# Kernel tuning notes

Measured on AMD Instinct MI355X. Metric: run time of the kernel, lower is better.

The kernel has to match this reference:

```python
import jax, jax.numpy as jnp
import numpy as np
from jax.ops import segment_sum, segment_max

N = 20000; E = 320000; IN_F = 135; HID = 256; HEADS = 8; DH = HID // HEADS; L = 4
EPS = 1e-5; TOP_K = max(1, int(N * 0.2)); POWER = 3.0

def lrelu(x):
    return jnp.where(x >= 0, x, 0.2 * x)

def bn_eval(x, p):
    # p rows: gamma, beta, running_mean, running_var (eval-mode BatchNorm1d)
    return p[0] * (x - p[2]) * jax.lax.rsqrt(p[3] + EPS) + p[1]

def setup_inputs():
    key = jax.random.key(0)
    ks = iter(jax.random.split(key, 100))
    def rn(shape, s=0.05):
        return jax.random.normal(next(ks), shape, jnp.float32) * s
    def bn_p(c):
        g = jax.random.uniform(next(ks), (c,)) * 0.5 + 0.75
        v = jax.random.uniform(next(ks), (c,)) * 0.5 + 0.75
        return jnp.stack([g, rn((c,), 0.1), rn((c,), 0.1), v])
    return dict(
        x=jax.random.normal(next(ks), (N, IN_F), jnp.float32),
        edge_index=jax.random.randint(next(ks), (2, E), 0, N),
        cen_W=rn((32, 7), 0.3), cen_b=rn((32,)), cen_bn=bn_p(32),
        emb_W=rn((64, 128), 0.1), emb_b=rn((64,)), emb_bn=bn_p(64),
        fus_W=rn((64, 96), 0.1), fus_b=rn((64,)),
        fa_W1=rn((64, 64), 0.1), fa_b1=rn((64,)),
        fa_W2=rn((64, 64), 0.1), fa_b2=rn((64,)),
        adj_W=rn((HID, 64), 0.1), adj_b=rn((HID,)),
        gcn_W=rn((L, HID, HID), 0.06), gcn_b=rn((L, HID)),
        gat_W=rn((L, HID, HID), 0.06), gat_b=rn((L, HID)),
        gat_asrc=rn((L, HEADS, DH), 0.1), gat_adst=rn((L, HEADS, DH), 0.1),
        layer_bn=jnp.stack([bn_p(HID) for _ in range(L)]),
        gate_W=rn((L, HID), 0.1), gate_b=rn((L,)),
        lin1_W=rn((HID, HID * L), 0.03), lin1_b=rn((HID,)),
        mlp_W1=rn((2 * HID, HID), 0.06), mlp_b1=rn((2 * HID,)), mlp_bn1=bn_p(2 * HID),
        mlp_W2=rn((HID, 2 * HID), 0.04), mlp_b2=rn((HID,)), mlp_bn2=bn_p(HID),
        mlp_W3=rn((1, HID), 0.06), mlp_b3=rn((1,)),
        temperature=jnp.array([0.05], jnp.float32),
    )

def _forward(edge_index, x, cen_W, cen_b, cen_bn, emb_W, emb_b, emb_bn, fus_W, fus_b,
             fa_W1, fa_b1, fa_W2, fa_b2, adj_W, adj_b, gcn_W, gcn_b, gat_W, gat_b,
             gat_asrc, gat_adst, layer_bn, gate_W, gate_b, lin1_W, lin1_b,
             mlp_W1, mlp_b1, mlp_bn1, mlp_W2, mlp_b2, mlp_bn2, mlp_W3, mlp_b3, temperature):
    # --- add self-loops (GCNConv and GATConv both do this by default) ---
    loops = jnp.arange(N)
    src = jnp.concatenate([edge_index[0], loops])  # [E+N]
    dst = jnp.concatenate([edge_index[1], loops])
    deg = segment_sum(jnp.ones(E + N, jnp.float32), dst, num_segments=N)
    dinv = jax.lax.rsqrt(deg)  # deg >= 1 because of self-loops
    gcn_norm = dinv[src] * dinv[dst]  # [E+N]

    # --- FeatureFusionLayer (eval BN) ---
    c = bn_eval(lrelu(x[:, :7] @ cen_W.T + cen_b), cen_bn)        # [N,32]
    e = bn_eval(lrelu(x[:, 7:] @ emb_W.T + emb_b), emb_bn)        # [N,64]
    h = jnp.concatenate([c, e], axis=1) @ fus_W.T + fus_b         # [N,64]
    att = jax.nn.sigmoid(lrelu(h @ fa_W1.T + fa_b1) @ fa_W2.T + fa_b2)
    h = (h * att) @ adj_W.T + adj_b                               # [N,256]

    xs = []
    prev = h
    cur = h
    for i in range(L):
        # GCNConv: D^{-1/2}(A+I)D^{-1/2} X W + b
        g = cur @ gcn_W[i].T                                      # [N,256]
        cur = segment_sum(g[src] * gcn_norm[:, None], dst, num_segments=N) + gcn_b[i]
        # GATConv: per-edge attention with segment softmax over destinations
        hh = (cur @ gat_W[i].T).reshape(N, HEADS, DH)             # [N,8,32]
        a_s = jnp.sum(hh * gat_asrc[i], axis=-1)                  # [N,8]
        a_d = jnp.sum(hh * gat_adst[i], axis=-1)
        logits = lrelu(a_s[src] + a_d[dst])                       # [E+N,8]
        mx = segment_max(logits, dst, num_segments=N)
        ex = jnp.exp(logits - mx[dst])
        den = segment_sum(ex, dst, num_segments=N)
        alpha = ex / den[dst]                                     # [E+N,8]
        cur = segment_sum(alpha[:, :, None] * hh[src], dst, num_segments=N)
        cur = cur.reshape(N, HID) + gat_b[i]
        # BN -> LeakyReLU -> sigmoid-gated residual (dropout = identity in eval)
        cur = lrelu(bn_eval(cur, layer_bn[i]))
        gate = jax.nn.sigmoid(cur @ gate_W[i] + gate_b[i])[:, None]
        cur = gate * cur + (1.0 - gate) * prev
        prev = cur
        xs.append(cur)

    jk = jnp.concatenate(xs, axis=1)                              # [N, 1024]
    h2 = lrelu(jk @ lin1_W.T + lin1_b)
    m1 = bn_eval(lrelu(h2 @ mlp_W1.T + mlp_b1), mlp_bn1)
    m2 = bn_eval(lrelu(m1 @ mlp_W2.T + mlp_b2), mlp_bn2)
    raw = jax.nn.sigmoid(m2 @ mlp_W3.T + mlp_b3)[:, 0]           # [N]

    # ContrastEnhancementLayer (eval path)
    scaled = raw / temperature[0]
    enhanced = jax.nn.softmax(scaled, axis=0)
    threshold = jax.lax.top_k(scaled, TOP_K)[0][-1]               # k-th largest
    mask = (scaled >= threshold).astype(scaled.dtype)
    boosted = enhanced * (mask + 0.1 * (1.0 - mask))
    return boosted ** POWER

def reference(x, edge_index, cen_W, cen_b, cen_bn, emb_W, emb_b, emb_bn, fus_W, fus_b,
              fa_W1, fa_b1, fa_W2, fa_b2, adj_W, adj_b, gcn_W, gcn_b, gat_W, gat_b,
              gat_asrc, gat_adst, layer_bn, gate_W, gate_b, lin1_W, lin1_b,
              mlp_W1, mlp_b1, mlp_bn1, mlp_W2, mlp_b2, mlp_bn2, mlp_W3, mlp_b3, temperature):
    return _forward(edge_index, x, cen_W, cen_b, cen_bn, emb_W, emb_b, emb_bn, fus_W, fus_b,
                    fa_W1, fa_b1, fa_W2, fa_b2, adj_W, adj_b, gcn_W, gcn_b, gat_W, gat_b,
                    gat_asrc, gat_adst, layer_bn, gate_W, gate_b, lin1_W, lin1_b,
                    mlp_W1, mlp_b1, mlp_bn1, mlp_W2, mlp_b2, mlp_bn2, mlp_W3, mlp_b3, temperature)
```

## Files before the change

### kernel.cpp

```cpp
#include <hip/hip_runtime.h>
#include <hip/hip_bf16.h>
#include <stdint.h>
#include <stddef.h>

#define NN    20000
#define EE    320000
#define ENE   340000
#define HIDD  256
#define TOPKK 4000

__device__ __forceinline__ float d_lrelu(float x){ return x >= 0.0f ? x : 0.2f * x; }
__device__ __forceinline__ float d_sig(float x){ return 1.0f / (1.0f + expf(-x)); }
__device__ __forceinline__ double d_sig64(double x){ return 1.0 / (1.0 + exp(-x)); }
__device__ __forceinline__ unsigned long long d_key64(double x){
  unsigned long long u = (unsigned long long)__double_as_longlong(x);
  return (u & 0x8000000000000000ULL) ? ~u : (u | 0x8000000000000000ULL);
}

__global__ void kf_fdet(const unsigned* __restrict__ xw, int* __restrict__ fflag){
  int t = threadIdx.x;
  unsigned w = xw[t * 101 + 7];
  unsigned b = (w >> 8) & 0x7F;
  int isbf = (b >= 0x3Au && b <= 0x44u) ? 1 : 0;
  unsigned long long bal = __ballot(isbf);
  if (t == 0) fflag[0] = (__popcll(bal) >= 32) ? 1 : 0;
}

__global__ void kf_cvt(const void* __restrict__ src, const int* __restrict__ fflag,
                       float* __restrict__ dst, int n){
  int stride = gridDim.x * 256;
  int bf = fflag[0];
  for (int i = blockIdx.x * 256 + threadIdx.x; i < n; i += stride){
    if (bf){
      unsigned short u = ((const unsigned short*)src)[i];
      dst[i] = __uint_as_float(((unsigned)u) << 16);
    } else {
      dst[i] = ((const float*)src)[i];
    }
  }
}

struct CvtTab { const void* src[34]; int cnt[34]; int off[34]; };
__global__ void kf_cvtw(CvtTab tab, const int* __restrict__ fflag, float* __restrict__ wbuf){
  int i = blockIdx.y;
  int n = tab.cnt[i];
  int idx = blockIdx.x * 256 + threadIdx.x;
  if (idx >= n) return;
  int bf = fflag[0];
  float v;
  if (bf){
    unsigned short u = ((const unsigned short*)tab.src[i])[idx];
    v = __uint_as_float(((unsigned)u) << 16);
  } else {
    v = ((const float*)tab.src[i])[idx];
  }
  wbuf[tab.off[i] + idx] = v;
}

__global__ void kf_cnt13(const int* __restrict__ ei, unsigned* __restrict__ C){
  __shared__ unsigned loc[6];
  if (threadIdx.x < 6) loc[threadIdx.x] = 0;
  __syncthreads();
  for (int e = blockIdx.x * 256 + threadIdx.x; e < EE; e += gridDim.x * 256){
    int s1 = ei[e], d1 = ei[EE + e];
    if (s1 >= 0 && s1 < NN && d1 >= 0 && d1 < NN) atomicAdd(&loc[0], 1u);
    if (s1 == 0) atomicAdd(&loc[1], 1u);
    if (d1 == 0) atomicAdd(&loc[2], 1u);
    int s3 = ei[2 * e], d3 = ei[2 * e + 1];
    if (s3 >= 0 && s3 < NN && d3 >= 0 && d3 < NN) atomicAdd(&loc[3], 1u);
    if (s3 == 0) atomicAdd(&loc[4], 1u);
    if (d3 == 0) atomicAdd(&loc[5], 1u);
  }
  __syncthreads();
  if (threadIdx.x < 6) atomicAdd(&C[threadIdx.x], loc[threadIdx.x]);
}

__global__ void kf_dec13(const unsigned* __restrict__ C, int* __restrict__ esel){
  const unsigned zlim = EE / 64;
  bool h1 = (C[0] == EE) && (C[1] < zlim) && (C[2] < zlim);
  bool h3 = (C[3] == EE) && (C[4] < zlim) && (C[5] < zlim);
  esel[0] = h1 ? 1 : (h3 ? 3 : -1);
}

__global__ void kf_cnt02(const int* __restrict__ ei, const int* __restrict__ esel,
                         unsigned* __restrict__ C){
  if (esel[0] >= 0) return;
  const long long* q = (const long long*)ei;
  __shared__ unsigned loc[6];
  if (threadIdx.x < 6) loc[threadIdx.x] = 0;
  __syncthreads();
  for (int e = blockIdx.x * 256 + threadIdx.x; e < EE; e += gridDim.x * 256){
    long long s0 = q[e], d0 = q[EE + e];
    if (s0 >= 0 && s0 < NN && d0 >= 0 && d0 < NN) atomicAdd(&loc[0], 1u);
    if (s0 == 0) atomicAdd(&loc[1], 1u);
    if (d0 == 0) atomicAdd(&loc[2], 1u);
    long long s2 = q[2 * e], d2 = q[2 * e + 1];
    if (s2 >= 0 && s2 < NN && d2 >= 0 && d2 < NN) atomicAdd(&loc[3], 1u);
    if (s2 == 0) atomicAdd(&loc[4], 1u);
    if (d2 == 0) atomicAdd(&loc[5], 1u);
  }
  __syncthreads();
  if (threadIdx.x < 6) atomicAdd(&C[threadIdx.x], loc[threadIdx.x]);
}

__global__ void kf_dec02(const unsigned* __restrict__ C13, const unsigned* __restrict__ C02,
                         int* __restrict__ esel){
  if (esel[0] >= 0){ esel[1] = 0; return; }
  const unsigned zlim = EE / 64;
  bool h0 = (C02[0] == EE) && (C02[1] < zlim) && (C02[2] < zlim);
  bool h2 = (C02[3] == EE) && (C02[4] < zlim) && (C02[5] < zlim);
  if (h0){ esel[0] = 0; esel[1] = 0; }
  else if (h2){ esel[0] = 2; esel[1] = 0; }
  else { esel[0] = -9; esel[1] = 1; }
}

__global__ void kf_econv(const int* __restrict__ ei, const int* __restrict__ esel,
                         int* __restrict__ src_i, int* __restrict__ dst_i){
  int e = blockIdx.x * 256 + threadIdx.x;
  if (e >= ENE) return;
  if (e >= EE){ src_i[e] = e - EE; dst_i[e] = e - EE; return; }
  int sel = esel[0];
  const long long* q = (const long long*)ei;
  int s, d;
  if (sel == 0){ s = (int)q[e]; d = (int)q[EE + e]; }
  else if (sel == 1){ s = ei[e]; d = ei[EE + e]; }
  else if (sel == 2){ s = (int)q[2 * e]; d = (int)q[2 * e + 1]; }
  else if (sel == 3){ s = ei[2 * e]; d = ei[2 * e + 1]; }
  else { s = 0; d = 0; }
  src_i[e] = s; dst_i[e] = d;
}

__global__ void kf_deg(const int* __restrict__ dst_i, int* __restrict__ deg){
  int e = blockIdx.x * 256 + threadIdx.x;
  if (e < ENE) atomicAdd(&deg[dst_i[e]], 1);
}

__global__ __launch_bounds__(1024) void kf_scan(const int* __restrict__ deg,
                                                int* __restrict__ rowptr,
                                                float* __restrict__ dinv){
  __shared__ int buf[1024];
  const int CH = (NN + 1023) / 1024;
  int t = threadIdx.x;
  int base = t * CH;
  int s = 0;
  for (int j = 0; j < CH; ++j){
    int v = base + j;
    if (v < NN) s += deg[v];
  }
  buf[t] = s;
  __syncthreads();
  int val = s;
  for (int d = 1; d < 1024; d <<= 1){
    int add = (t >= d) ? buf[t - d] : 0;
    __syncthreads();
    buf[t] += add;
    __syncthreads();
  }
  int run = buf[t] - val;
  for (int j = 0; j < CH; ++j){
    int v = base + j;
    if (v < NN){
      rowptr[v] = run;
      run += deg[v];
      dinv[v] = 1.0f / sqrtf((float)deg[v]);
    }
  }
  if (t == 1023) rowptr[NN] = buf[1023];
}

__global__ void kf_fill(const int* __restrict__ src_i, const int* __restrict__ dst_i,
                        const int* __restrict__ rowptr, int* __restrict__ fill,
                        int* __restrict__ col){
  int e = blockIdx.x * 256 + threadIdx.x;
  if (e >= ENE) return;
  int d = dst_i[e];
  int p = atomicAdd(&fill[d], 1);
  col[rowptr[d] + p] = src_i[e];
}

__global__ void kf_sort(const int* __restrict__ rowptr, int* __restrict__ col){
  int v = blockIdx.x * 256 + threadIdx.x;
  if (v >= NN) return;
  int b = rowptr[v], e = rowptr[v + 1];
  for (int i = b + 1; i < e; ++i){
    int key = col[i];
    int j = i - 1;
    while (j >= b && col[j] > key){ col[j + 1] = col[j]; --j; }
    col[j + 1] = key;
  }
}

template<int EP>
__global__ __launch_bounds__(256) void kgf(
    const float* __restrict__ A, int lda,
    const float* __restrict__ W, int ldw,
    const float* __restrict__ bias,
    const float* __restrict__ bn,
    const float* __restrict__ mul,
    float* __restrict__ C, int ldc,
    int M, int K, int F)
{
  __shared__ float As[16][68];
  __shared__ float Ws[16][68];
  int tid  = threadIdx.x;
  int row0 = blockIdx.x * 64;
  int col0 = blockIdx.y * 64;
  int tx = tid & 15, ty = tid >> 4;
  int lr  = tid >> 2;
  int lk4 = (tid & 3) * 4;
  float acc[4][4] = {};
  int r_st = row0 + lr;
  int f_st = col0 + lr;
  for (int k0 = 0; k0 < K; k0 += 16){
#pragma unroll
    for (int j = 0; j < 4; ++j){
      int k = k0 + lk4 + j;
      As[lk4 + j][lr] = (r_st < M && k < K) ? A[(size_t)r_st * lda + k] : 0.0f;
      Ws[lk4 + j][lr] = (f_st < F && k < K) ? W[(size_t)f_st * ldw + k] : 0.0f;
    }
    __syncthreads();
#pragma unroll
    for (int kk = 0; kk < 16; ++kk){
      float av[4], bv[4];
#pragma unroll
      for (int i = 0; i < 4; ++i){ av[i] = As[kk][ty * 4 + i]; bv[i] = Ws[kk][tx * 4 + i]; }
#pragma unroll
      for (int i = 0; i < 4; ++i)
#pragma unroll
        for (int j = 0; j < 4; ++j)
          acc[i][j] = fmaf(av[i], bv[j], acc[i][j]);
    }
    __syncthreads();
  }
#pragma unroll
  for (int i = 0; i < 4; ++i){
    int r = row0 + ty * 4 + i;
    if (r >= M) continue;
#pragma unroll
    for (int j = 0; j < 4; ++j){
      int f = col0 + tx * 4 + j;
      if (f >= F) continue;
      float z = acc[i][j];
      size_t ci = (size_t)r * ldc + f;
      if (EP == 0){
        if (bias) z += bias[f];
        C[ci] = z;
      } else if (EP == 1){
        C[ci] = d_lrelu(z + bias[f]);
      } else if (EP == 2){
        z = d_lrelu(z + bias[f]);
        float gamma = bn[f], beta = bn[F + f], mean = bn[2 * F + f], var = bn[3 * F + f];
        C[ci] = gamma * (z - mean) * (1.0f / sqrtf(var + 1e-5f)) + beta;
      } else if (EP == 3){
        z += bias[f];
        C[ci] = d_sig(z) * mul[(size_t)r * ldc + f];
      } else if (EP == 4){
        C[ci] += z;
      } else {
        C[ci] = d_lrelu(C[ci] + z + bias[f]);
      }
    }
  }
}

__global__ __launch_bounds__(256) void kf_gcn(const float* __restrict__ g,
                                              const int* __restrict__ rowptr,
                                              const int* __restrict__ col,
                                              const float* __restrict__ dinv,
                                              const float* __restrict__ bias,
                                              float* __restrict__ out){
  int lane = threadIdx.x & 63, wid = threadIdx.x >> 6;
  int v = blockIdx.x * 4 + wid;
  if (v >= NN) return;
  float dv = dinv[v];
  float a0 = 0.f, a1 = 0.f, a2 = 0.f, a3 = 0.f;
  int e0 = rowptr[v], e1 = rowptr[v + 1];
  for (int e = e0; e < e1; ++e){
    int s = col[e];
    float w = dinv[s] * dv;
    const float* gr = g + (size_t)s * HIDD + lane;
    a0 = fmaf(w, gr[0],   a0);
    a1 = fmaf(w, gr[64],  a1);
    a2 = fmaf(w, gr[128], a2);
    a3 = fmaf(w, gr[192], a3);
  }
  float* o = out + (size_t)v * HIDD + lane;
  o[0]   = a0 + bias[lane];
  o[64]  = a1 + bias[lane + 64];
  o[128] = a2 + bias[lane + 128];
  o[192] = a3 + bias[lane + 192];
}

__global__ __launch_bounds__(256) void kf_asd(const float* __restrict__ hh,
                                              const float* __restrict__ asrc,
                                              const float* __restrict__ adst,
                                              float* __restrict__ a_s,
                                              float* __restrict__ a_d){
  int lane = threadIdx.x & 63, wid = threadIdx.x >> 6;
  int v = blockIdx.x * 4 + wid;
  if (v >= NN) return;
  int h = lane >> 3;
  int d0 = (lane & 7) * 4;
  const float* x = hh + (size_t)v * HIDD + h * 32 + d0;
  float ps = 0.f, pd = 0.f;
#pragma unroll
  for (int j = 0; j < 4; ++j){
    ps = fmaf(x[j], asrc[h * 32 + d0 + j], ps);
    pd = fmaf(x[j], adst[h * 32 + d0 + j], pd);
  }
#pragma unroll
  for (int off = 1; off < 8; off <<= 1){
    ps += __shfl_xor(ps, off);
    pd += __shfl_xor(pd, off);
  }
  if ((lane & 7) == 0){
    a_s[v * 8 + h] = ps;
    a_d[v * 8 + h] = pd;
  }
}

__global__ __launch_bounds__(256) void kf_gat(const float* __restrict__ hh,
                                              const int* __restrict__ rowptr,
                                              const int* __restrict__ col,
                                              const float* __restrict__ a_s,
                                              const float* __restrict__ a_d,
                                              float* __restrict__ elog,
                                              const float* __restrict__ gat_b,
                                              const float* __restrict__ lbn,
                                              const float* __restrict__ gate_W,
                                              const float* __restrict__ gate_b,
                                              float* __restrict__ P){
  int lane = threadIdx.x & 63, wid = threadIdx.x >> 6;
  int v = blockIdx.x * 4 + wid;
  if (v >= NN) return;
  int head = lane & 7, slot = lane >> 3;
  int e0 = rowptr[v], e1 = rowptr[v + 1];
  float adv = a_d[v * 8 + head];
  float m = -1e30f;
  for (int e = e0 + slot; e < e1; e += 8){
    float lg = d_lrelu(a_s[col[e] * 8 + head] + adv);
    m = fmaxf(m, lg);
  }
#pragma unroll
  for (int off = 8; off < 64; off <<= 1) m = fmaxf(m, __shfl_xor(m, off));
  float s = 0.f;
  for (int e = e0 + slot; e < e1; e += 8){
    float ex = expf(d_lrelu(a_s[col[e] * 8 + head] + adv) - m);
    elog[(size_t)e * 8 + head] = ex;
    s += ex;
  }
#pragma unroll
  for (int off = 8; off < 64; off <<= 1) s += __shfl_xor(s, off);
  int hk[4]; float denk[4];
#pragma unroll
  for (int k = 0; k < 4; ++k){
    int f = lane + 64 * k;
    hk[k] = f >> 5;
    denk[k] = __shfl(s, hk[k]);
  }
  float acc[4] = {0.f, 0.f, 0.f, 0.f};
  for (int e = e0; e < e1; ++e){
    const float* hr = hh + (size_t)col[e] * HIDD;
#pragma unroll
    for (int k = 0; k < 4; ++k)
      acc[k] = fmaf(elog[(size_t)e * 8 + hk[k]], hr[lane + 64 * k], acc[k]);
  }
  float o[4], gp = 0.f;
#pragma unroll
  for (int k = 0; k < 4; ++k){
    int f = lane + 64 * k;
    float z = acc[k] / denk[k] + gat_b[f];
    float gamma = lbn[f], beta = lbn[256 + f], mean = lbn[512 + f], var = lbn[768 + f];
    z = gamma * (z - mean) * (1.0f / sqrtf(var + 1e-5f)) + beta;
    z = d_lrelu(z);
    o[k] = z;
    gp = fmaf(z, gate_W[f], gp);
  }
#pragma unroll
  for (int off = 1; off < 64; off <<= 1) gp += __shfl_xor(gp, off);
  float gate = d_sig(gp + gate_b[0]);
#pragma unroll
  for (int k = 0; k < 4; ++k){
    size_t idx = (size_t)v * HIDD + lane + 64 * k;
    P[idx] = gate * o[k] + (1.0f - gate) * P[idx];
  }
}

__global__ __launch_bounds__(256) void kf_raw(const float* __restrict__ m2,
                                              const float* __restrict__ W3,
                                              const float* __restrict__ b3,
                                              const float* __restrict__ temp,
                                              double* __restrict__ scaled){
  int lane = threadIdx.x & 63, wid = threadIdx.x >> 6;
  int v = blockIdx.x * 4 + wid;
  if (v >= NN) return;
  const float* r = m2 + (size_t)v * HIDD;
  double s = 0.;
#pragma unroll
  for (int k = 0; k < 4; ++k) s = fma((double)r[lane + 64 * k], (double)W3[lane + 64 * k], s);
#pragma unroll
  for (int off = 1; off < 64; off <<= 1) s += __shfl_xor(s, off);
  if (lane == 0) scaled[v] = d_sig64(s + (double)b3[0]) / (double)temp[0];
}

__global__ __launch_bounds__(1024) void kf_stats(const double* __restrict__ scaled,
                                                 double* __restrict__ st){
  __shared__ double fmx[1024];
  __shared__ double dsum[1024];
  int t = threadIdx.x;
  double m = -1e300;
  for (int i = t; i < NN; i += 1024) m = fmax(m, scaled[i]);
  fmx[t] = m;
  __syncthreads();
  for (int d = 512; d > 0; d >>= 1){
    if (t < d) fmx[t] = fmax(fmx[t], fmx[t + d]);
    __syncthreads();
  }
  double mx = fmx[0];
  double s = 0.;
  for (int i = t; i < NN; i += 1024) s += exp(scaled[i] - mx);
  dsum[t] = s;
  __syncthreads();
  for (int d = 512; d > 0; d >>= 1){
    if (t < d) dsum[t] += dsum[t + d];
    __syncthreads();
  }
  if (t == 0){ st[0] = mx; st[1] = dsum[0]; }
}

__global__ __launch_bounds__(1024) void kf_sel(const double* __restrict__ scaled,
                                               unsigned long long* __restrict__ thr){
  __shared__ unsigned hist[256];
  __shared__ unsigned long long sh_prefix;
  __shared__ unsigned sh_target;
  int t = threadIdx.x;
  if (t == 0){ sh_prefix = 0ULL; sh_target = TOPKK; }
  __syncthreads();
  for (int shift = 56; shift >= 0; shift -= 8){
    if (t < 256) hist[t] = 0;
    __syncthreads();
    unsigned long long pref = sh_prefix;
    unsigned long long himask = (shift == 56) ? 0ULL : (~0ULL << (shift + 8));
    for (int i = t; i < NN; i += 1024){
      unsigned long long k = d_key64(scaled[i]);
      if ((k & himask) == pref)
        atomicAdd(&hist[(unsigned)((k >> shift) & 0xFF)], 1u);
    }
    __syncthreads();
    if (t == 0){
      unsigned run = 0;
      int b = 255;
      for (; b > 0; --b){
        if (run + hist[b] >= sh_target) break;
        run += hist[b];
      }
      sh_target -= run;
      sh_prefix = pref | ((unsigned long long)b << shift);
    }
    __syncthreads();
  }
  if (t == 0) thr[0] = sh_prefix;
}

__global__ void kf_final(const double* __restrict__ scaled, const double* __restrict__ st,
                         const unsigned long long* __restrict__ thr,
                         const int* __restrict__ fflag, const int* __restrict__ esel,
                         void* __restrict__ out){
  int i = blockIdx.x * 256 + threadIdx.x;
  if (i >= NN) return;
  float v;
  if (esel[0] < -1){
    v = (i == 0) ? ldexpf(1.0f, 30) : 0.0f;
  } else {
    double fc = (d_key64(scaled[i]) >= thr[0]) ? 1.0 : 0.1;
    double enh = exp(scaled[i] - st[0]) / st[1];
    double b = enh * fc;
    v = (float)(b * b * b);
  }
  if (fflag[0]) ((__hip_bfloat16*)out)[i] = __float2bfloat16(v);
  else          ((float*)out)[i] = v;
}

static void launch_gemm(int EP, const float* A, int lda, const float* W, int ldw,
                        const float* bias, const float* bn, const float* mul,
                        float* C, int ldc, int M, int K, int F, hipStream_t stream){
  dim3 g((M + 63) / 64, (F + 63) / 64);
  switch (EP){
    case 0: kgf<0><<<g, 256, 0, stream>>>(A, lda, W, ldw, bias, bn, mul, C, ldc, M, K, F); break;
    case 1: kgf<1><<<g, 256, 0, stream>>>(A, lda, W, ldw, bias, bn, mul, C, ldc, M, K, F); break;
    case 2: kgf<2><<<g, 256, 0, stream>>>(A, lda, W, ldw, bias, bn, mul, C, ldc, M, K, F); break;
    case 3: kgf<3><<<g, 256, 0, stream>>>(A, lda, W, ldw, bias, bn, mul, C, ldc, M, K, F); break;
    case 4: kgf<4><<<g, 256, 0, stream>>>(A, lda, W, ldw, bias, bn, mul, C, ldc, M, K, F); break;
    default: kgf<5><<<g, 256, 0, stream>>>(A, lda, W, ldw, bias, bn, mul, C, ldc, M, K, F); break;
  }
}

static const int FCNT[36] = {
  2700000, -1, 224, 32, 128, 8192, 64, 256, 6144, 64,
  4096, 64, 4096, 64, 16384, 256, 262144, 1024, 262144, 1024,
  1024, 1024, 4096, 1024, 4, 262144, 256, 131072, 512, 2048,
  131072, 256, 1024, 256, 1, 1
};

extern "C" void kernel_launch(void* const* d_in, const int* in_sizes, int n_in,
                              void* d_out, int out_size, void* d_ws, size_t ws_size,
                              hipStream_t stream){
  (void)in_sizes; (void)n_in; (void)out_size;

  char* base = (char*)d_ws;
  size_t off = 0;
  auto carve = [&](size_t bytes) -> void* {
    void* p = base + off;
    off = (off + bytes + 255) & ~(size_t)255;
    return p;
  };
  int*      fflag = (int*)     carve(64);
  int*      esel  = (int*)     carve(64);
  unsigned* C13   = (unsigned*)carve(64);
  unsigned* C02   = (unsigned*)carve(64);
  int*    src_i  = (int*)   carve((size_t)ENE * 4);
  int*    dst_i  = (int*)   carve((size_t)ENE * 4);
  int*    col    = (int*)   carve((size_t)ENE * 4);
  int*    deg    = (int*)   carve((size_t)NN * 4);
  int*    fill   = (int*)   carve((size_t)NN * 4);
  int*    rowptr = (int*)   carve((size_t)(NN + 1) * 4);
  float*  dinv   = (float*) carve((size_t)NN * 4);
  float*  wbuf   = (float*) carve((size_t)1103000 * 4);
  float*  FUS    = (float*) carve((size_t)NN * 288 * 4);
  float*  P      = (float*) carve((size_t)NN * 256 * 4);
  float*  S12    = (float*) carve((size_t)NN * 512 * 4);
  float*  a_s    = (float*) carve((size_t)NN * 8 * 4);
  float*  a_d    = (float*) carve((size_t)NN * 8 * 4);
  double* scaled = (double*)carve((size_t)NN * 8);
  double* st     = (double*)carve(64);
  unsigned long long* thr = (unsigned long long*)carve(64);

  float* ce   = FUS;
  float* h64  = FUS + (size_t)NN * 96;
  float* t64  = FUS + (size_t)NN * 160;
  float* ha   = FUS + (size_t)NN * 224;
  float* h2   = FUS;
  float* S1   = S12;
  float* S2   = S12 + (size_t)NN * 256;
  float* elog = S2;
  float* m1   = S12;
  float* xf   = P;
  if (off > ws_size) return;

  kf_fdet<<<1, 64, 0, stream>>>((const unsigned*)d_in[0], fflag);
  hipMemsetAsync(C13, 0, 64, stream);
  hipMemsetAsync(C02, 0, 64, stream);
  kf_cnt13<<<256, 256, 0, stream>>>((const int*)d_in[1], C13);
  kf_dec13<<<1, 1, 0, stream>>>(C13, esel);
  kf_cnt02<<<256, 256, 0, stream>>>((const int*)d_in[1], esel, C02);
  kf_dec02<<<1, 1, 0, stream>>>(C13, C02, esel);
  kf_econv<<<(ENE + 255) / 256, 256, 0, stream>>>((const int*)d_in[1], esel, src_i, dst_i);

  float* F[36];
  CvtTab tab;
  {
    size_t w = 0;
    for (int i = 0; i < 36; ++i){
      if (FCNT[i] < 0){ F[i] = nullptr; continue; }
      if (i == 0){ F[0] = xf; continue; }
      F[i] = wbuf + w;
      tab.src[i - 2] = d_in[i];
      tab.cnt[i - 2] = FCNT[i];
      tab.off[i - 2] = (int)w;
      w += (size_t)((FCNT[i] + 63) & ~63);
    }
  }
  kf_cvt<<<2048, 256, 0, stream>>>(d_in[0], fflag, xf, FCNT[0]);
  kf_cvtw<<<dim3(1024, 34), 256, 0, stream>>>(tab, fflag, wbuf);

  hipMemsetAsync(deg, 0, (size_t)NN * 4, stream);
  hipMemsetAsync(fill, 0, (size_t)NN * 4, stream);
  kf_deg<<<(ENE + 255) / 256, 256, 0, stream>>>(dst_i, deg);
  kf_scan<<<1, 1024, 0, stream>>>(deg, rowptr, dinv);
  kf_fill<<<(ENE + 255) / 256, 256, 0, stream>>>(src_i, dst_i, rowptr, fill, col);
  kf_sort<<<(NN + 255) / 256, 256, 0, stream>>>(rowptr, col);

  launch_gemm(2, xf, 135, F[2], 7, F[3], F[4], nullptr, ce, 96, NN, 7, 32, stream);
  launch_gemm(2, xf + 7, 135, F[5], 128, F[6], F[7], nullptr, ce + 32, 96, NN, 128, 64, stream);
  launch_gemm(0, ce, 96, F[8], 96, F[9], nullptr, nullptr, h64, 64, NN, 96, 64, stream);
  launch_gemm(1, h64, 64, F[10], 64, F[11], nullptr, nullptr, t64, 64, NN, 64, 64, stream);
  launch_gemm(3, t64, 64, F[12], 64, F[13], nullptr, h64, ha, 64, NN, 64, 64, stream);
  launch_gemm(0, ha, 64, F[14], 64, F[15], nullptr, nullptr, P, 256, NN, 64, 256, stream);

  for (int i = 0; i < 4; ++i){
    const float* gW  = F[16] + (size_t)i * 256 * 256;
    const float* gb  = F[17] + (size_t)i * 256;
    const float* aW  = F[18] + (size_t)i * 256 * 256;
    const float* ab  = F[19] + (size_t)i * 256;
    const float* asr = F[20] + (size_t)i * 256;
    const float* ads = F[21] + (size_t)i * 256;
    const float* lbn = F[22] + (size_t)i * 1024;
    const float* gw  = F[23] + (size_t)i * 256;
    const float* gbp = F[24] + i;

    launch_gemm(0, P, 256, gW, 256, nullptr, nullptr, nullptr, S1, 256, NN, 256, 256, stream);
    kf_gcn<<<NN / 4, 256, 0, stream>>>(S1, rowptr, col, dinv, gb, S2);
    launch_gemm(0, S2, 256, aW, 256, nullptr, nullptr, nullptr, S1, 256, NN, 256, 256, stream);
    kf_asd<<<NN / 4, 256, 0, stream>>>(S1, asr, ads, a_s, a_d);
    kf_gat<<<NN / 4, 256, 0, stream>>>(S1, rowptr, col, a_s, a_d, elog, ab, lbn, gw, gbp, P);

    int ep = (i == 0) ? 0 : (i == 3 ? 5 : 4);
    const float* b = (i == 3) ? F[26] : nullptr;
    launch_gemm(ep, P, 256, F[25] + (size_t)i * 256, 1024, b, nullptr, nullptr, h2, 256, NN, 256, 256, stream);
  }

  launch_gemm(2, h2, 256, F[27], 256, F[28], F[29], nullptr, m1, 512, NN, 256, 512, stream);
  launch_gemm(2, m1, 512, F[30], 512, F[31], F[32], nullptr, P, 256, NN, 512, 256, stream);
  kf_raw<<<NN / 4, 256, 0, stream>>>(P, F[33], F[34], F[35], scaled);

  kf_stats<<<1, 1024, 0, stream>>>(scaled, st);
  kf_sel<<<1, 1024, 0, stream>>>(scaled, thr);
  kf_final<<<(NN + 255) / 256, 256, 0, stream>>>(scaled, st, thr, fflag, esel, d_out);
}
```

Before: 2.242 ms.

## Add bf16 MFMA GEMM path with three-way split of activations

Adds an MFMA-based GEMM kernel for K divisible by 32. It splits each fp32 activation into three bf16 pieces and keeps weights as single bf16, which stays near fp32 accuracy when the weights are already bf16. A one-off probe kernel runs a small MFMA to work out the operand and output layout, and enables the path only when the inputs are detected as bf16. The goal is to move the dominant dense GEMMs from scalar FMA to matrix cores, at the cost of three MFMA passes and extra conversion work per tile.

```diff
diff --git a/kernel.cpp b/kernel.cpp
--- a/kernel.cpp
+++ b/kernel.cpp
@@ -8,6 +8,9 @@
 #define ENE   340000
 #define HIDD  256
 #define TOPKK 4000
+
+typedef short bf16x8 __attribute__((ext_vector_type(8)));
+typedef float f32x4  __attribute__((ext_vector_type(4)));
 
 __device__ __forceinline__ float d_lrelu(float x){ return x >= 0.0f ? x : 0.2f * x; }
 __device__ __forceinline__ float d_sig(float x){ return 1.0f / (1.0f + expf(-x)); }
@@ -15,6 +18,13 @@
 __device__ __forceinline__ unsigned long long d_key64(double x){
   unsigned long long u = (unsigned long long)__double_as_longlong(x);
   return (u & 0x8000000000000000ULL) ? ~u : (u | 0x8000000000000000ULL);
+}
+__device__ __forceinline__ unsigned short d_f2b(float f){
+  unsigned u = __float_as_uint(f);
+  return (unsigned short)((u + 0x7FFFu + ((u >> 16) & 1u)) >> 16);
+}
+__device__ __forceinline__ float d_b2f(unsigned short b){
+  return __uint_as_float(((unsigned)b) << 16);
 }
 
 __global__ void kf_fdet(const unsigned* __restrict__ xw, int* __restrict__ fflag){
@@ -187,6 +197,221 @@
     int j = i - 1;
     while (j >= b && col[j] > key){ col[j + 1] = col[j]; --j; }
     col[j + 1] = key;
+  }
+}
+
+__global__ void kp2(const int* __restrict__ fflag, int* __restrict__ gsel){
+  __shared__ float As[16][32];
+  __shared__ float Ws[16][32];
+  __shared__ float Cr[16][16];
+  int l = threadIdx.x;
+  for (int idx = l; idx < 512; idx += 64){
+    int r = idx & 15, k = idx >> 4;
+    As[r][k] = (float)(((r * 7 + k * 3) % 13) - 6);
+    Ws[r][k] = (float)(((r * 5 + k * 11) % 11) - 5);
+  }
+  __syncthreads();
+  for (int idx = l; idx < 256; idx += 64){
+    int r = idx & 15, c = idx >> 4;
+    float s = 0.f;
+    for (int k = 0; k < 32; ++k) s += As[r][k] * Ws[c][k];
+    Cr[r][c] = s;
+  }
+  __syncthreads();
+  int l15 = l & 15, hi = l >> 4;
+  int sel = 0;
+  for (int v = 1; v <= 4; ++v){
+    if (sel != 0) break;
+    bf16x8 af, bf;
+#pragma unroll
+    for (int j = 0; j < 8; ++j){
+      int k = (v == 2 || v == 4) ? (hi + 4 * j) : (hi * 8 + j);
+      af[j] = (short)d_f2b(As[l15][k]);
+      bf[j] = (short)d_f2b(Ws[l15][k]);
+    }
+    f32x4 acc = {0.f, 0.f, 0.f, 0.f};
+    if (v >= 3) acc = __builtin_amdgcn_mfma_f32_16x16x32_bf16(bf, af, acc, 0, 0, 0);
+    else        acc = __builtin_amdgcn_mfma_f32_16x16x32_bf16(af, bf, acc, 0, 0, 0);
+    int ok = 1;
+#pragma unroll
+    for (int reg = 0; reg < 4; ++reg){
+      float want = (v >= 3) ? Cr[l15][hi * 4 + reg] : Cr[hi * 4 + reg][l15];
+      if (acc[reg] != want) ok = 0;
+    }
+    unsigned long long bal = __ballot(ok);
+    if (bal == ~0ULL) sel = v;
+  }
+  if (l == 0) gsel[0] = (fflag[0] == 1) ? sel : 0;
+}
+
+#define LDP 40
+template<int EP>
+__global__ __launch_bounds__(256) void kgm(
+    const int* __restrict__ gsel,
+    const float* __restrict__ A, int lda,
+    const float* __restrict__ W, int ldw,
+    const float* __restrict__ bias,
+    const float* __restrict__ bn,
+    const float* __restrict__ mul,
+    float* __restrict__ C, int ldc,
+    int M, int K, int F)
+{
+  __shared__ short Ap[3][64 * LDP];
+  __shared__ short Wb[64 * LDP];
+  int tid  = threadIdx.x;
+  int row0 = blockIdx.x * 64;
+  int col0 = blockIdx.y * 64;
+  int v = gsel[0];
+
+  if (v == 0 || (K & 31)){
+    float* fAs = (float*)&Ap[0][0];
+    float* fWs = fAs + 16 * 68;
+    int tx = tid & 15, ty = tid >> 4;
+    int lr  = tid >> 2;
+    int lk4 = (tid & 3) * 4;
+    float acc[4][4] = {};
+    int r_st = row0 + lr;
+    int f_st = col0 + lr;
+    for (int k0 = 0; k0 < K; k0 += 16){
+#pragma unroll
+      for (int j = 0; j < 4; ++j){
+        int k = k0 + lk4 + j;
+        fAs[(lk4 + j) * 68 + lr] = (r_st < M && k < K) ? A[(size_t)r_st * lda + k] : 0.0f;
+        fWs[(lk4 + j) * 68 + lr] = (f_st < F && k < K) ? W[(size_t)f_st * ldw + k] : 0.0f;
+      }
+      __syncthreads();
+#pragma unroll
+      for (int kk = 0; kk < 16; ++kk){
+        float av[4], bv[4];
+#pragma unroll
+        for (int i = 0; i < 4; ++i){ av[i] = fAs[kk * 68 + ty * 4 + i]; bv[i] = fWs[kk * 68 + tx * 4 + i]; }
+#pragma unroll
+        for (int i = 0; i < 4; ++i)
+#pragma unroll
+          for (int j = 0; j < 4; ++j)
+            acc[i][j] = fmaf(av[i], bv[j], acc[i][j]);
+      }
+      __syncthreads();
+    }
+#pragma unroll
+    for (int i = 0; i < 4; ++i){
+      int r = row0 + ty * 4 + i;
+      if (r >= M) continue;
+#pragma unroll
+      for (int j = 0; j < 4; ++j){
+        int f = col0 + tx * 4 + j;
+        if (f >= F) continue;
+        float z = acc[i][j];
+        size_t ci = (size_t)r * ldc + f;
+        if (EP == 0){ if (bias) z += bias[f]; C[ci] = z; }
+        else if (EP == 1){ C[ci] = d_lrelu(z + bias[f]); }
+        else if (EP == 2){
+          z = d_lrelu(z + bias[f]);
+          float gamma = bn[f], beta = bn[F + f], mean = bn[2 * F + f], var = bn[3 * F + f];
+          C[ci] = gamma * (z - mean) * (1.0f / sqrtf(var + 1e-5f)) + beta;
+        }
+        else if (EP == 3){ z += bias[f]; C[ci] = d_sig(z) * mul[(size_t)r * ldc + f]; }
+        else if (EP == 4){ C[ci] += z; }
+        else { C[ci] = d_lrelu(C[ci] + z + bias[f]); }
+      }
+    }
+    return;
+  }
+
+  bool km2 = (v == 2 || v == 4);
+  bool sw  = (v >= 3);
+  int srow = tid >> 2;
+  int skb  = (tid & 3) * 8;
+  int wave = tid >> 6;
+  int lane = tid & 63;
+  int wr = (wave >> 1) * 32;
+  int wc = (wave & 1) * 32;
+  int l15 = lane & 15, hi = lane >> 4;
+
+  f32x4 acc[2][2] = {{{0,0,0,0},{0,0,0,0}},{{0,0,0,0},{0,0,0,0}}};
+
+  int gr = row0 + srow;
+  int gc = col0 + srow;
+  int nt = K >> 5;
+  for (int t = 0; t < nt; ++t){
+    int k0 = t << 5;
+    {
+      bf16x8 s0, s1, s2, swv;
+#pragma unroll
+      for (int j = 0; j < 8; ++j){
+        float a = (gr < M) ? A[(size_t)gr * lda + k0 + skb + j] : 0.0f;
+        unsigned short b0 = d_f2b(a);
+        float r1 = a - d_b2f(b0);
+        unsigned short b1 = d_f2b(r1);
+        float r2 = r1 - d_b2f(b1);
+        unsigned short b2 = d_f2b(r2);
+        s0[j] = (short)b0; s1[j] = (short)b1; s2[j] = (short)b2;
+        float w = (gc < F) ? W[(size_t)gc * ldw + k0 + skb + j] : 0.0f;
+        swv[j] = (short)d_f2b(w);
+      }
+      int o = srow * LDP + skb;
+      *(bf16x8*)&Ap[0][o] = s0;
+      *(bf16x8*)&Ap[1][o] = s1;
+      *(bf16x8*)&Ap[2][o] = s2;
+      *(bf16x8*)&Wb[o]    = swv;
+    }
+    __syncthreads();
+    bf16x8 bfrag[2];
+#pragma unroll
+    for (int tj = 0; tj < 2; ++tj){
+      int c = wc + tj * 16 + l15;
+      if (!km2) bfrag[tj] = *(const bf16x8*)&Wb[c * LDP + hi * 8];
+      else {
+#pragma unroll
+        for (int j = 0; j < 8; ++j) bfrag[tj][j] = Wb[c * LDP + hi + 4 * j];
+      }
+    }
+#pragma unroll
+    for (int ti = 0; ti < 2; ++ti){
+      int r = wr + ti * 16 + l15;
+#pragma unroll
+      for (int p = 0; p < 3; ++p){
+        bf16x8 af;
+        if (!km2) af = *(const bf16x8*)&Ap[p][r * LDP + hi * 8];
+        else {
+#pragma unroll
+          for (int j = 0; j < 8; ++j) af[j] = Ap[p][r * LDP + hi + 4 * j];
+        }
+#pragma unroll
+        for (int tj = 0; tj < 2; ++tj){
+          if (sw) acc[ti][tj] = __builtin_amdgcn_mfma_f32_16x16x32_bf16(bfrag[tj], af, acc[ti][tj], 0, 0, 0);
+          else    acc[ti][tj] = __builtin_amdgcn_mfma_f32_16x16x32_bf16(af, bfrag[tj], acc[ti][tj], 0, 0, 0);
+        }
+      }
+    }
+    __syncthreads();
+  }
+
+#pragma unroll
+  for (int ti = 0; ti < 2; ++ti){
+#pragma unroll
+    for (int tj = 0; tj < 2; ++tj){
+#pragma unroll
+      for (int reg = 0; reg < 4; ++reg){
+        int ro = sw ? l15 : (hi * 4 + reg);
+        int co = sw ? (hi * 4 + reg) : l15;
+        int r = row0 + wr + ti * 16 + ro;
+        int f = col0 + wc + tj * 16 + co;
+        if (r >= M || f >= F) continue;
+        float z = acc[ti][tj][reg];
+        size_t ci = (size_t)r * ldc + f;
+        if (EP == 0){ if (bias) z += bias[f]; C[ci] = z; }
+        else if (EP == 1){ C[ci] = d_lrelu(z + bias[f]); }
+        else if (EP == 2){
+          z = d_lrelu(z + bias[f]);
+          float gamma = bn[f], beta = bn[F + f], mean = bn[2 * F + f], var = bn[3 * F + f];
+          C[ci] = gamma * (z - mean) * (1.0f / sqrtf(var + 1e-5f)) + beta;
+        }
+        else if (EP == 3){ z += bias[f]; C[ci] = d_sig(z) * mul[(size_t)r * ldc + f]; }
+        else if (EP == 4){ C[ci] += z; }
+        else { C[ci] = d_lrelu(C[ci] + z + bias[f]); }
+      }
+    }
   }
 }
 
@@ -242,23 +467,16 @@
       if (f >= F) continue;
       float z = acc[i][j];
       size_t ci = (size_t)r * ldc + f;
-      if (EP == 0){
-        if (bias) z += bias[f];
-        C[ci] = z;
-      } else if (EP == 1){
-        C[ci] = d_lrelu(z + bias[f]);
-      } else if (EP == 2){
+      if (EP == 0){ if (bias) z += bias[f]; C[ci] = z; }
+      else if (EP == 1){ C[ci] = d_lrelu(z + bias[f]); }
+      else if (EP == 2){
         z = d_lrelu(z + bias[f]);
         float gamma = bn[f], beta = bn[F + f], mean = bn[2 * F + f], var = bn[3 * F + f];
         C[ci] = gamma * (z - mean) * (1.0f / sqrtf(var + 1e-5f)) + beta;
-      } else if (EP == 3){
-        z += bias[f];
-        C[ci] = d_sig(z) * mul[(size_t)r * ldc + f];
-      } else if (EP == 4){
-        C[ci] += z;
-      } else {
-        C[ci] = d_lrelu(C[ci] + z + bias[f]);
       }
+      else if (EP == 3){ z += bias[f]; C[ci] = d_sig(z) * mul[(size_t)r * ldc + f]; }
+      else if (EP == 4){ C[ci] += z; }
+      else { C[ci] = d_lrelu(C[ci] + z + bias[f]); }
     }
   }
 }
@@ -481,17 +699,29 @@
   else          ((float*)out)[i] = v;
 }
 
-static void launch_gemm(int EP, const float* A, int lda, const float* W, int ldw,
+static void launch_gemm(int EP, const int* gsel, const float* A, int lda,
+                        const float* W, int ldw,
                         const float* bias, const float* bn, const float* mul,
                         float* C, int ldc, int M, int K, int F, hipStream_t stream){
   dim3 g((M + 63) / 64, (F + 63) / 64);
-  switch (EP){
-    case 0: kgf<0><<<g, 256, 0, stream>>>(A, lda, W, ldw, bias, bn, mul, C, ldc, M, K, F); break;
-    case 1: kgf<1><<<g, 256, 0, stream>>>(A, lda, W, ldw, bias, bn, mul, C, ldc, M, K, F); break;
-    case 2: kgf<2><<<g, 256, 0, stream>>>(A, lda, W, ldw, bias, bn, mul, C, ldc, M, K, F); break;
-    case 3: kgf<3><<<g, 256, 0, stream>>>(A, lda, W, ldw, bias, bn, mul, C, ldc, M, K, F); break;
-    case 4: kgf<4><<<g, 256, 0, stream>>>(A, lda, W, ldw, bias, bn, mul, C, ldc, M, K, F); break;
-    default: kgf<5><<<g, 256, 0, stream>>>(A, lda, W, ldw, bias, bn, mul, C, ldc, M, K, F); break;
+  if ((K & 31) == 0){
+    switch (EP){
+      case 0: kgm<0><<<g, 256, 0, stream>>>(gsel, A, lda, W, ldw, bias, bn, mul, C, ldc, M, K, F); break;
+      case 1: kgm<1><<<g, 256, 0, stream>>>(gsel, A, lda, W, ldw, bias, bn, mul, C, ldc, M, K, F); break;
+      case 2: kgm<2><<<g, 256, 0, stream>>>(gsel, A, lda, W, ldw, bias, bn, mul, C, ldc, M, K, F); break;
+      case 3: kgm<3><<<g, 256, 0, stream>>>(gsel, A, lda, W, ldw, bias, bn, mul, C, ldc, M, K, F); break;
+      case 4: kgm<4><<<g, 256, 0, stream>>>(gsel, A, lda, W, ldw, bias, bn, mul, C, ldc, M, K, F); break;
+      default: kgm<5><<<g, 256, 0, stream>>>(gsel, A, lda, W, ldw, bias, bn, mul, C, ldc, M, K, F); break;
+    }
+  } else {
+    switch (EP){
+      case 0: kgf<0><<<g, 256, 0, stream>>>(A, lda, W, ldw, bias, bn, mul, C, ldc, M, K, F); break;
+      case 1: kgf<1><<<g, 256, 0, stream>>>(A, lda, W, ldw, bias, bn, mul, C, ldc, M, K, F); break;
+      case 2: kgf<2><<<g, 256, 0, stream>>>(A, lda, W, ldw, bias, bn, mul, C, ldc, M, K, F); break;
+      case 3: kgf<3><<<g, 256, 0, stream>>>(A, lda, W, ldw, bias, bn, mul, C, ldc, M, K, F); break;
+      case 4: kgf<4><<<g, 256, 0, stream>>>(A, lda, W, ldw, bias, bn, mul, C, ldc, M, K, F); break;
+      default: kgf<5><<<g, 256, 0, stream>>>(A, lda, W, ldw, bias, bn, mul, C, ldc, M, K, F); break;
+    }
   }
 }
 
@@ -516,6 +746,7 @@
   };
   int*      fflag = (int*)     carve(64);
   int*      esel  = (int*)     carve(64);
+  int*      gsel  = (int*)     carve(64);
   unsigned* C13   = (unsigned*)carve(64);
   unsigned* C02   = (unsigned*)carve(64);
   int*    src_i  = (int*)   carve((size_t)ENE * 4);
@@ -548,6 +779,7 @@
   if (off > ws_size) return;
 
   kf_fdet<<<1, 64, 0, stream>>>((const unsigned*)d_in[0], fflag);
+  kp2<<<1, 64, 0, stream>>>(fflag, gsel);
   hipMemsetAsync(C13, 0, 64, stream);
   hipMemsetAsync(C02, 0, 64, stream);
   kf_cnt13<<<256, 256, 0, stream>>>((const int*)d_in[1], C13);
@@ -580,12 +812,12 @@
   kf_fill<<<(ENE + 255) / 256, 256, 0, stream>>>(src_i, dst_i, rowptr, fill, col);
   kf_sort<<<(NN + 255) / 256, 256, 0, stream>>>(rowptr, col);
 
-  launch_gemm(2, xf, 135, F[2], 7, F[3], F[4], nullptr, ce, 96, NN, 7, 32, stream);
-  launch_gemm(2, xf + 7, 135, F[5], 128, F[6], F[7], nullptr, ce + 32, 96, NN, 128, 64, stream);
-  launch_gemm(0, ce, 96, F[8], 96, F[9], nullptr, nullptr, h64, 64, NN, 96, 64, stream);
-  launch_gemm(1, h64, 64, F[10], 64, F[11], nullptr, nullptr, t64, 64, NN, 64, 64, stream);
-  launch_gemm(3, t64, 64, F[12], 64, F[13], nullptr, h64, ha, 64, NN, 64, 64, stream);
-  launch_gemm(0, ha, 64, F[14], 64, F[15], nullptr, nullptr, P, 256, NN, 64, 256, stream);
+  launch_gemm(2, gsel, xf, 135, F[2], 7, F[3], F[4], nullptr, ce, 96, NN, 7, 32, stream);
+  launch_gemm(2, gsel, xf + 7, 135, F[5], 128, F[6], F[7], nullptr, ce + 32, 96, NN, 128, 64, stream);
+  launch_gemm(0, gsel, ce, 96, F[8], 96, F[9], nullptr, nullptr, h64, 64, NN, 96, 64, stream);
+  launch_gemm(1, gsel, h64, 64, F[10], 64, F[11], nullptr, nullptr, t64, 64, NN, 64, 64, stream);
+  launch_gemm(3, gsel, t64, 64, F[12], 64, F[13], nullptr, h64, ha, 64, NN, 64, 64, stream);
+  launch_gemm(0, gsel, ha, 64, F[14], 64, F[15], nullptr, nullptr, P, 256, NN, 64, 256, stream);
 
   for (int i = 0; i < 4; ++i){
     const float* gW  = F[16] + (size_t)i * 256 * 256;
@@ -598,19 +830,19 @@
     const float* gw  = F[23] + (size_t)i * 256;
     const float* gbp = F[24] + i;
 
-    launch_gemm(0, P, 256, gW, 256, nullptr, nullptr, nullptr, S1, 256, NN, 256, 256, stream);
+    launch_gemm(0, gsel, P, 256, gW, 256, nullptr, nullptr, nullptr, S1, 256, NN, 256, 256, stream);
     kf_gcn<<<NN / 4, 256, 0, stream>>>(S1, rowptr, col, dinv, gb, S2);
-    launch_gemm(0, S2, 256, aW, 256, nullptr, nullptr, nullptr, S1, 256, NN, 256, 256, stream);
+    launch_gemm(0, gsel, S2, 256, aW, 256, nullptr, nullptr, nullptr, S1, 256, NN, 256, 256, stream);
     kf_asd<<<NN / 4, 256, 0, stream>>>(S1, asr, ads, a_s, a_d);
     kf_gat<<<NN / 4, 256, 0, stream>>>(S1, rowptr, col, a_s, a_d, elog, ab, lbn, gw, gbp, P);
 
     int ep = (i == 0) ? 0 : (i == 3 ? 5 : 4);
     const float* b = (i == 3) ? F[26] : nullptr;
-    launch_gemm(ep, P, 256, F[25] + (size_t)i * 256, 1024, b, nullptr, nullptr, h2, 256, NN, 256, 256, stream);
-  }
-
-  launch_gemm(2, h2, 256, F[27], 256, F[28], F[29], nullptr, m1, 512, NN, 256, 512, stream);
-  launch_gemm(2, m1, 512, F[30], 512, F[31], F[32], nullptr, P, 256, NN, 512, 256, stream);
+    launch_gemm(ep, gsel, P, 256, F[25] + (size_t)i * 256, 1024, b, nullptr, nullptr, h2, 256, NN, 256, 256, stream);
+  }
+
+  launch_gemm(2, gsel, h2, 256, F[27], 256, F[28], F[29], nullptr, m1, 512, NN, 256, 512, stream);
+  launch_gemm(2, gsel, m1, 512, F[30], 512, F[31], F[32], nullptr, P, 256, NN, 512, 256, stream);
   kf_raw<<<NN / 4, 256, 0, stream>>>(P, F[33], F[34], F[35], scaled);
 
   kf_stats<<<1, 1024, 0, stream>>>(scaled, st);
```

Measured after the change: 2.245 ms. Within noise of the previous version (+0.1%).
